# Kernel optimization log

Hardware: AMD Instinct MI355X
Metric: run time of the kernel (lower is better)

Reference implementation:

```python
import jax, jax.numpy as jnp
import numpy as np

B, T, S = 64, 256, 512          # batch, decode steps, source length
IN, H, P, C = 512, 512, 256, 512  # in_size, rnn hidden, ctx_proj_size, ctx_size


def setup_inputs() -> dict:
    key = jax.random.key(0)
    ks = jax.random.split(key, 10)
    def n(k, sh, s=0.05):
        return jax.random.normal(k, sh, dtype=jnp.float32) * s
    return {
        "dec_input": n(ks[0], (B, T, IN), 1.0),
        "ctx": n(ks[1], (B, S, C), 1.0),
        "ctx_mask": jnp.ones((B, S), jnp.float32),
        # LSTMCell layer 0: input = in_size + ctx_proj_size (input feeding)
        "Wih0": n(ks[2], (4 * H, IN + P)),
        "Whh0": n(ks[3], (4 * H, H)),
        "bih0": jnp.zeros((4 * H,), jnp.float32),
        "bhh0": jnp.zeros((4 * H,), jnp.float32),
        # LSTMCell layer 1
        "Wih1": n(ks[4], (4 * H, H)),
        "Whh1": n(ks[5], (4 * H, H)),
        "bih1": jnp.zeros((4 * H,), jnp.float32),
        "bhh1": jnp.zeros((4 * H,), jnp.float32),
        # bilinear (Luong general) attention weight
        "Watt": n(ks[6], (H, C)),
        # ctx projection: Linear(rnn_size + att.out_features -> ctx_proj_size)
        "Wproj": n(ks[7], (P, H + C)),
        "bproj": jnp.zeros((P,), jnp.float32),
    }


def _lstm_cell(x, h, c, Wih, Whh, bih, bhh):
    # PyTorch LSTMCell gate order: i, f, g, o
    g = x @ Wih.T + bih + h @ Whh.T + bhh
    i, f, gg, o = jnp.split(g, 4, axis=-1)
    c_new = jax.nn.sigmoid(f) * c + jax.nn.sigmoid(i) * jnp.tanh(gg)
    h_new = jax.nn.sigmoid(o) * jnp.tanh(c_new)
    return h_new, c_new


def reference(dec_input, ctx, ctx_mask, Wih0, Whh0, bih0, bhh0,
              Wih1, Whh1, bih1, bhh1, Watt, Wproj, bproj):
    Bn = dec_input.shape[0]
    neg = (ctx_mask - 1.0) * 1e9  # additive mask: 0 where valid, -1e9 where pad

    def step(carry, x_t):
        h0, c0, h1, c1, feed = carry
        # input feeding at layer 0
        x = jnp.concatenate([x_t, feed], axis=1)
        h0, c0 = _lstm_cell(x, h0, c0, Wih0, Whh0, bih0, bhh0)
        h1, c1 = _lstm_cell(h0, h1, c1, Wih1, Whh1, bih1, bhh1)
        # attention on last layer (att_nth_layer == -1)
        q = h1 @ Watt                                   # [B, C]
        score = jnp.einsum('bc,bsc->bs', q, ctx) + neg  # [B, S]
        alpha = jax.nn.softmax(score, axis=-1)
        ectx = jnp.einsum('bs,bsc->bc', alpha, ctx)     # expected context [B, C]
        # ctx projection with tanh (scale_src = scale_tgt = 1.0)
        res = jnp.tanh(jnp.concatenate([h1, ectx], axis=1) @ Wproj.T + bproj)
        return (h0, c0, h1, c1, res), (res, alpha)

    z = lambda d: jnp.zeros((Bn, d), jnp.float32)
    init = (z(H), z(H), z(H), z(H), z(P))
    _, (dec_out, att_w) = jax.lax.scan(step, init, jnp.swapaxes(dec_input, 0, 1))
    # dec_output [B, T, P], attention weights [B, T, S]
    return jnp.swapaxes(dec_out, 0, 1), jnp.swapaxes(att_w, 0, 1)
```

## Files before the change

### kernel.cpp

```cpp
#include <hip/hip_runtime.h>
#include <math.h>

#define B  64
#define T  256
#define S  512
#define IN 512
#define H  512
#define P  256
#define C  512

typedef _Float16 f16x8 __attribute__((ext_vector_type(8)));
typedef float    f32x4 __attribute__((ext_vector_type(4)));
typedef unsigned short u16x8 __attribute__((ext_vector_type(8)));

#define MFMA16(a, b, c) __builtin_amdgcn_mfma_f32_16x16x32_f16(a, b, c, 0, 0, 0)

#define O_C0      0
#define O_C1      131072
#define O_H0F0    262144
#define O_H1F0    524288
#define O_FEEDF   786432
#define O_H1F32   851968
#define O_XF0     983040
#define O_Q       1245184
#define O_PS      1376256
#define O_PSP     1378304
#define O_PEA     1509376
#define O_BCAT0   2557952
#define O_BCAT1   2566144
#define O_WPROJT  2574336
#define O_W0F     3622912
#define O_W1F     14108672
#define O_WATTF   22497280
#define O_CTXH    23545856
#define O_CNTA    57100288
#define O_CNT3    57104384
#define O_H0F1N   57169920
#define O_H1F1N   57300992
#define O_XF1N    57432064

__device__ __forceinline__ float sigm(float x) { return 1.f / (1.f + __expf(-x)); }

__device__ __forceinline__ void split2(float v, unsigned short& hi, unsigned short& lo)
{
    _Float16 h = (_Float16)v;
    float r = (v - (float)h) * 4096.f;
    _Float16 l2 = (_Float16)r;
    union { _Float16 f; unsigned short u; } a, b2;
    a.f = h; b2.f = l2;
    hi = a.u; lo = b2.u;
}

__device__ __forceinline__ unsigned short f2h(float v)
{
    union { _Float16 f; unsigned short u; } x;
    x.f = (_Float16)v;
    return x.u;
}

__device__ __forceinline__ float h2f(unsigned short u)
{
    union { unsigned short u; _Float16 f; } x;
    x.u = u;
    return (float)x.f;
}

__device__ __forceinline__ int frag_us(int r, int k)
{
    return ((((k >> 5) * 4 + (r >> 4)) * 64 + ((k >> 3) & 3) * 16 + (r & 15)) * 16) + (k & 7);
}

__device__ __forceinline__ void gemm_core(
    const unsigned short* A0, int n0, const unsigned short* A1, int n1,
    const unsigned short* A2, const unsigned short* Wf, int nks, int ct,
    float* red, int tid)
{
    const int l = tid & 63, kh = tid >> 6;
    f32x4 acch[4] = {};
    f32x4 accl[4] = {};
    const int KQ = nks >> 3;
#pragma unroll 2
    for (int i = 0; i < KQ; ++i) {
        const int ks = kh * KQ + i;
        const unsigned short* ap; int ksl;
        if (ks < n0)           { ap = A0; ksl = ks; }
        else if (ks < n0 + n1) { ap = A1; ksl = ks - n0; }
        else                   { ap = A2; ksl = ks - n0 - n1; }
        const f16x8 b = *(const f16x8*)(Wf + ((long)(ct * nks + ks) * 64 + l) * 8);
#pragma unroll
        for (int mt = 0; mt < 4; ++mt) {
            const f16x8* app = (const f16x8*)(ap + (((ksl * 4 + mt) * 64 + l) * 16));
            const f16x8 ah = app[0];
            const f16x8 al = app[1];
            acch[mt] = MFMA16(ah, b, acch[mt]);
            accl[mt] = MFMA16(al, b, accl[mt]);
        }
    }
#pragma unroll
    for (int mt = 0; mt < 4; ++mt) {
        f32x4 v = acch[mt] + accl[mt] * (1.f / 4096.f);
        *(f32x4*)&red[(kh * 64 + l) * 20 + mt * 4] = v;
    }
}

__device__ __forceinline__ void lstm_epi(const float* red, const float* bias,
                                         float* cbuf, unsigned short* hfrag,
                                         float* hf32_out, int ct, int tid)
{
    const int b = tid & 63, hl = tid >> 6;
    float g4[4];
#pragma unroll
    for (int g = 0; g < 4; ++g) {
        const int col = hl * 4 + g;
        const int li  = ((b & 15) >> 2) * 16 + col;
        const int ri  = (b >> 4) * 4 + (b & 3);
        float v = bias[ct * 16 + col];
#pragma unroll
        for (int k2 = 0; k2 < 8; ++k2) v += red[(k2 * 64 + li) * 20 + ri];
        g4[g] = v;
    }
    const int hg = ct * 4 + hl;
    const float cold = cbuf[b * H + hg];
    const float cn = sigm(g4[1]) * cold + sigm(g4[0]) * tanhf(g4[2]);
    cbuf[b * H + hg] = cn;
    const float hn = sigm(g4[3]) * tanhf(cn);
    unsigned short hi, lo; split2(hn, hi, lo);
    const int fu = frag_us(b, hg);
    hfrag[fu]     = hi;
    hfrag[fu + 8] = lo;
    if (hf32_out) hf32_out[b * H + hg] = hn;
}

__global__ __launch_bounds__(512)
void k1_kernel(char* __restrict__ wsb, const float* __restrict__ dec_input, int t)
{
    __shared__ float lds[10240];
    const int bid = blockIdx.x, tid = threadIdx.x;
    const int cur = t & 1, nxt = cur ^ 1;
    unsigned short* h0f[2] = {(unsigned short*)(wsb + O_H0F0), (unsigned short*)(wsb + O_H0F1N)};
    unsigned short* xf[2]  = {(unsigned short*)(wsb + O_XF0),  (unsigned short*)(wsb + O_XF1N)};

    if (bid < 128) {
        gemm_core(xf[cur], 16, (unsigned short*)(wsb + O_FEEDF), 8, h0f[cur],
                  (const unsigned short*)(wsb + O_W0F), 40, bid, lds, tid);
        __syncthreads();
        if (tid < 256)
            lstm_epi(lds, (const float*)(wsb + O_BCAT0), (float*)(wsb + O_C0),
                     h0f[nxt], nullptr, bid, tid);
    } else if (t + 1 < T) {
        const int idx = (bid - 128) * 512 + tid;
        const int bb = idx >> 9, k = idx & 511;
        unsigned short hi, lo;
        split2(dec_input[((long)bb * T + (t + 1)) * IN + k], hi, lo);
        unsigned short* dst = xf[nxt];
        const int fu = frag_us(bb, k);
        dst[fu]     = hi;
        dst[fu + 8] = lo;
    }
}

__global__ __launch_bounds__(512)
void k2_kernel(char* __restrict__ wsb, int t)
{
    __shared__ float lds[10240];
    const int bid = blockIdx.x, tid = threadIdx.x;
    const int cur = t & 1, nxt = cur ^ 1;
    unsigned short* h0f[2] = {(unsigned short*)(wsb + O_H0F0), (unsigned short*)(wsb + O_H0F1N)};
    unsigned short* h1f[2] = {(unsigned short*)(wsb + O_H1F0), (unsigned short*)(wsb + O_H1F1N)};

    gemm_core(h0f[nxt], 16, h1f[cur], 16, nullptr,
              (const unsigned short*)(wsb + O_W1F), 32, bid, lds, tid);
    __syncthreads();
    if (tid < 256)
        lstm_epi(lds, (const float*)(wsb + O_BCAT1), (float*)(wsb + O_C1),
                 h1f[nxt], (float*)(wsb + O_H1F32), bid, tid);
}

__global__ __launch_bounds__(512)
void q_kernel(char* __restrict__ wsb, int t)
{
    __shared__ float lds[10240];
    const int bid = blockIdx.x, tid = threadIdx.x;
    const int nxt = (t & 1) ^ 1;
    unsigned short* h1f[2] = {(unsigned short*)(wsb + O_H1F0), (unsigned short*)(wsb + O_H1F1N)};
    float* qbuf = (float*)(wsb + O_Q);

    gemm_core(h1f[nxt], 16, nullptr, 0, nullptr,
              (const unsigned short*)(wsb + O_WATTF), 16, bid, lds, tid);
    __syncthreads();
    if (tid < 256) {
        const int b = tid & 63, cl = tid >> 6;
        float4 vv;
#pragma unroll
        for (int c2 = 0; c2 < 4; ++c2) {
            const int col = cl * 4 + c2;
            const int li  = ((b & 15) >> 2) * 16 + col;
            const int ri  = (b >> 4) * 4 + (b & 3);
            float v = 0.f;
#pragma unroll
            for (int k2 = 0; k2 < 8; ++k2) v += lds[(k2 * 64 + li) * 20 + ri];
            ((float*)&vv)[c2] = v;
        }
        *(float4*)(qbuf + b * C + bid * 16 + cl * 4) = vv;
    }
}

__global__ __launch_bounds__(512)
void qattn_kernel(char* __restrict__ wsb, const float* __restrict__ mask, int t)
{
    __shared__ float qs[512];
    __shared__ unsigned short tile[32 * 520];
    __shared__ float scl[64];

    const int bid = blockIdx.x, tid = threadIdx.x;
    const int b = bid >> 3, ei = bid & 7;
    const float* qbuf = (const float*)(wsb + O_Q);
    const unsigned short* ctxh = (const unsigned short*)(wsb + O_CTXH);
    float* pS  = (float*)(wsb + O_PSP);
    float* Ps  = (float*)(wsb + O_PS);
    float* Pea = (float*)(wsb + O_PEA);

    const unsigned short* cb16 = ctxh + ((long)b * S + ei * 64) * C;
    u16x8 creg[4];
#pragma unroll
    for (int it = 0; it < 4; ++it)
        creg[it] = *(const u16x8*)(cb16 + (long)(it * 512 + tid) * 8);

    if (tid < 128) ((float4*)qs)[tid] = ((const float4*)(qbuf + (long)b * C))[tid];
    __syncthreads();

    const int row = tid >> 4;
    const int ch  = tid & 15;
    float qv[32];
#pragma unroll
    for (int j = 0; j < 32; ++j) qv[j] = qs[ch * 32 + j];

    float eacc = 0.f;
#pragma unroll
    for (int tt = 0; tt < 2; ++tt) {
#pragma unroll
        for (int it = 0; it < 4; ++it) {
            const int i = it * 512 + tid;
            const int r = (i >> 6) & 31, c8 = i & 63;
            *(u16x8*)&tile[r * 520 + c8 * 8] = creg[it];
        }
        __syncthreads();
        if (tt == 0) {
#pragma unroll
            for (int it = 0; it < 4; ++it)
                creg[it] = *(const u16x8*)(cb16 + 32 * 512 + (long)(it * 512 + tid) * 8);
        }
        float part = 0.f;
#pragma unroll
        for (int j4 = 0; j4 < 4; ++j4) {
            const u16x8 cv = *(const u16x8*)&tile[row * 520 + ch * 32 + j4 * 8];
#pragma unroll
            for (int m = 0; m < 8; ++m)
                part = fmaf(h2f(cv[m]), qv[j4 * 8 + m], part);
        }
        part += __shfl_xor(part, 1);
        part += __shfl_xor(part, 2);
        part += __shfl_xor(part, 4);
        part += __shfl_xor(part, 8);
        if (ch == 0) {
            const int srow = ei * 64 + tt * 32 + row;
            const float sc = part + (mask[(long)b * S + srow] - 1.f) * 1e9f;
            const float p  = __expf(sc - 20.f);
            scl[tt * 32 + row] = p;
            pS[(long)b * S + srow] = p;
        }
        __syncthreads();
#pragma unroll 8
        for (int s = 0; s < 32; ++s)
            eacc = fmaf(scl[tt * 32 + s], h2f(tile[s * 520 + tid]), eacc);
        __syncthreads();
    }

    Pea[(long)bid * 512 + tid] = eacc;
    if (tid < 64) {
        float v = scl[tid];
#pragma unroll
        for (int off = 32; off; off >>= 1) v += __shfl_xor(v, off);
        if (tid == 0) Ps[bid] = v;
    }
}

__global__ __launch_bounds__(512)
void mergeproj_kernel(char* __restrict__ wsb, const float* __restrict__ bproj,
                      float* __restrict__ out, int t)
{
    __shared__ float ectx[512];
    __shared__ float h1l[512];
    __shared__ float red[512];

    const int b = blockIdx.x, tid = threadIdx.x;
    const float* Ps  = (const float*)(wsb + O_PS);
    const float* Pea = (const float*)(wsb + O_PEA);
    const float* pS  = (const float*)(wsb + O_PSP);
    const float* h1f32 = (const float*)(wsb + O_H1F32);
    const unsigned short* Wph = (const unsigned short*)(wsb + O_WPROJT);
    unsigned short* feedf = (unsigned short*)(wsb + O_FEEDF);

    float* dec_out = out;
    float* att_out = out + (long)B * T * P;

    float gs = 0.f;
#pragma unroll
    for (int j = 0; j < 8; ++j) gs += Ps[b * 8 + j];
    const float inv = 1.f / gs;

    float v = 0.f;
#pragma unroll
    for (int j = 0; j < 8; ++j) v += Pea[(long)(b * 8 + j) * 512 + tid];
    ectx[tid] = v * inv;
    h1l[tid]  = h1f32[(long)b * H + tid];
    att_out[((long)b * T + t) * S + tid] = pS[(long)b * S + tid] * inv;
    __syncthreads();

    const int p = tid & 255, half = tid >> 8;
    const float* al = half ? ectx : h1l;
    const unsigned short* Wp = Wph + (long)(half * 512) * P + p;
    float acc = 0.f;
#pragma unroll 8
    for (int kk = 0; kk < 512; ++kk)
        acc = fmaf(al[kk], h2f(Wp[(long)kk * P]), acc);
    red[tid] = acc;
    __syncthreads();

    if (tid < 256) {
        float vv = red[tid] + red[tid + 256] + bproj[tid];
        vv = tanhf(vv);
        dec_out[((long)b * T + t) * P + tid] = vv;
        unsigned short hi, lo; split2(vv, hi, lo);
        const int fu = frag_us(b, tid);
        feedf[fu]     = hi;
        feedf[fu + 8] = lo;
    }
}

__global__ __launch_bounds__(256)
void prep_all(const float* __restrict__ dec_input,
              const float* __restrict__ Wih0, const float* __restrict__ Whh0,
              const float* __restrict__ bih0, const float* __restrict__ bhh0,
              const float* __restrict__ Wih1, const float* __restrict__ Whh1,
              const float* __restrict__ bih1, const float* __restrict__ bhh1,
              const float* __restrict__ Watt, const float* __restrict__ Wproj,
              const float* __restrict__ ctx,
              char* __restrict__ wsb)
{
    const int bid = blockIdx.x, tid = threadIdx.x;
    if (bid < 240) {
        float4 z = {0.f, 0.f, 0.f, 0.f};
        ((float4*)wsb)[bid * 256 + tid] = z;
    } else if (bid < 368) {
        const int idx = (bid - 240) * 256 + tid;
        const int bb = idx >> 9, k = idx & 511;
        unsigned short hi, lo;
        split2(dec_input[((long)bb * T) * IN + k], hi, lo);
        unsigned short* xf0 = (unsigned short*)(wsb + O_XF0);
        const int fu = frag_us(bb, k);
        xf0[fu] = hi; xf0[fu + 8] = lo;
    } else if (bid < 384) {
        const int idx = (bid - 368) * 256 + tid;
        if (idx < 2048) {
            const int p = idx, h = p >> 2, g = p & 3, orig = g * H + h;
            ((float*)(wsb + O_BCAT0))[p] = bih0[orig] + bhh0[orig];
        } else {
            const int p = idx - 2048, h = p >> 2, g = p & 3, orig = g * H + h;
            ((float*)(wsb + O_BCAT1))[p] = bih1[orig] + bhh1[orig];
        }
    } else if (bid < 512) {
        const int idx = (bid - 384) * 256 + tid;
        const int n = idx >> 6, k = (idx & 63) * 8;
        u16x8 hv;
#pragma unroll
        for (int j = 0; j < 8; ++j) hv[j] = f2h(Watt[(long)(k + j) * C + n]);
        unsigned short* Wf = (unsigned short*)(wsb + O_WATTF);
        const long base = ((long)((n >> 4) * 16 + (k >> 5)) * 64 + ((k >> 3) & 3) * 16 + (n & 15)) * 8;
        *(u16x8*)(Wf + base) = hv;
    } else if (bid < 1536) {
        const int idx = (bid - 512) * 256 + tid;
        const int k = idx >> 8, p = idx & 255;
        ((unsigned short*)(wsb + O_WPROJT))[k * P + p] = f2h(Wproj[(long)p * (H + C) + k]);
    } else if (bid < 2816) {
        const int idx = (bid - 1536) * 256 + tid;
        const int n = idx / 160, k8 = idx - n * 160;
        const int k = k8 * 8;
        const int h = n >> 2, g = n & 3, orig = g * H + h;
        const float* src = (k < IN + P) ? (Wih0 + (long)orig * (IN + P) + k)
                                        : (Whh0 + (long)orig * H + (k - (IN + P)));
        u16x8 hv;
#pragma unroll
        for (int j = 0; j < 8; ++j) hv[j] = f2h(src[j]);
        unsigned short* Wf = (unsigned short*)(wsb + O_W0F);
        const long base = ((long)((n >> 4) * 40 + (k >> 5)) * 64 + ((k >> 3) & 3) * 16 + (n & 15)) * 8;
        *(u16x8*)(Wf + base) = hv;
    } else if (bid < 3840) {
        const int idx = (bid - 2816) * 256 + tid;
        const int n = idx >> 7, k = (idx & 127) * 8;
        const int h = n >> 2, g = n & 3, orig = g * H + h;
        const float* src = (k < H) ? (Wih1 + (long)orig * H + k)
                                   : (Whh1 + (long)orig * H + (k - H));
        u16x8 hv;
#pragma unroll
        for (int j = 0; j < 8; ++j) hv[j] = f2h(src[j]);
        unsigned short* Wf = (unsigned short*)(wsb + O_W1F);
        const long base = ((long)((n >> 4) * 32 + (k >> 5)) * 64 + ((k >> 3) & 3) * 16 + (n & 15)) * 8;
        *(u16x8*)(Wf + base) = hv;
    } else if (bid < 7936) {
        const long idx = (long)(bid - 3840) * 256 + tid;
        const float* src = ctx + idx * 16;
        unsigned short* dst = (unsigned short*)(wsb + O_CTXH) + idx * 16;
        u16x8 o0, o1;
#pragma unroll
        for (int j = 0; j < 8; ++j) {
            o0[j] = f2h(src[j]);
            o1[j] = f2h(src[j + 8]);
        }
        *(u16x8*)dst       = o0;
        *(u16x8*)(dst + 8) = o1;
    } else {
        float4 z = {0.f, 0.f, 0.f, 0.f};
        ((float4*)(wsb + O_CNTA))[(bid - 7936) * 256 + tid] = z;
    }
}

extern "C" void kernel_launch(void* const* d_in, const int* in_sizes, int n_in,
                              void* d_out, int out_size, void* d_ws, size_t ws_size,
                              hipStream_t stream)
{
    (void)in_sizes; (void)n_in; (void)out_size; (void)ws_size;
    const float* dec_input = (const float*)d_in[0];
    const float* ctx       = (const float*)d_in[1];
    const float* mask      = (const float*)d_in[2];
    const float* Wih0      = (const float*)d_in[3];
    const float* Whh0      = (const float*)d_in[4];
    const float* bih0      = (const float*)d_in[5];
    const float* bhh0      = (const float*)d_in[6];
    const float* Wih1      = (const float*)d_in[7];
    const float* Whh1      = (const float*)d_in[8];
    const float* bih1      = (const float*)d_in[9];
    const float* bhh1      = (const float*)d_in[10];
    const float* Watt      = (const float*)d_in[11];
    const float* Wproj     = (const float*)d_in[12];
    const float* bproj     = (const float*)d_in[13];
    float* out = (float*)d_out;
    char*  wsb = (char*)d_ws;

    prep_all<<<7953, 256, 0, stream>>>(dec_input, Wih0, Whh0, bih0, bhh0,
                                       Wih1, Whh1, bih1, bhh1, Watt, Wproj,
                                       ctx, wsb);

    for (int t = 0; t < T; ++t) {
        k1_kernel<<<192, 512, 0, stream>>>(wsb, dec_input, t);
        k2_kernel<<<128, 512, 0, stream>>>(wsb, t);
        q_kernel<<<32, 512, 0, stream>>>(wsb, t);
        qattn_kernel<<<512, 512, 0, stream>>>(wsb, mask, t);
        mergeproj_kernel<<<64, 512, 0, stream>>>(wsb, bproj, out, t);
    }
}
```

Before: 13.92 ms.

## Precompute recurrent-independent LSTM gate partials off the critical path

```diff
diff --git a/kernel.cpp b/kernel.cpp
--- a/kernel.cpp
+++ b/kernel.cpp
@@ -30,11 +30,13 @@
 #define O_BCAT1   2566144
 #define O_WPROJT  2574336
 #define O_W0F     3622912
+#define O_PK1A    8865792
+#define O_PK1B    9390080
+#define O_PK2A    9914368
+#define O_PK2B    10438656
 #define O_W1F     14108672
 #define O_WATTF   22497280
 #define O_CTXH    23545856
-#define O_CNTA    57100288
-#define O_CNT3    57104384
 #define O_H0F1N   57169920
 #define O_H1F1N   57300992
 #define O_XF1N    57432064
@@ -72,8 +74,8 @@
 
 __device__ __forceinline__ void gemm_core(
     const unsigned short* A0, int n0, const unsigned short* A1, int n1,
-    const unsigned short* A2, const unsigned short* Wf, int nks, int ct,
-    float* red, int tid)
+    const unsigned short* A2, const unsigned short* Wf, int wnks, int wbase,
+    int nks, int ct, float* red, int tid)
 {
     const int l = tid & 63, kh = tid >> 6;
     f32x4 acch[4] = {};
@@ -86,7 +88,7 @@
         if (ks < n0)           { ap = A0; ksl = ks; }
         else if (ks < n0 + n1) { ap = A1; ksl = ks - n0; }
         else                   { ap = A2; ksl = ks - n0 - n1; }
-        const f16x8 b = *(const f16x8*)(Wf + ((long)(ct * nks + ks) * 64 + l) * 8);
+        const f16x8 b = *(const f16x8*)(Wf + ((long)(ct * wnks + wbase + ks) * 64 + l) * 8);
 #pragma unroll
         for (int mt = 0; mt < 4; ++mt) {
             const f16x8* app = (const f16x8*)(ap + (((ksl * 4 + mt) * 64 + l) * 16));
@@ -103,18 +105,35 @@
     }
 }
 
-__device__ __forceinline__ void lstm_epi(const float* red, const float* bias,
-                                         float* cbuf, unsigned short* hfrag,
-                                         float* hf32_out, int ct, int tid)
+__device__ __forceinline__ void part_store(const float* red, float* Pp,
+                                           int ct, int tid)
 {
     const int b = tid & 63, hl = tid >> 6;
-    float g4[4];
 #pragma unroll
     for (int g = 0; g < 4; ++g) {
         const int col = hl * 4 + g;
         const int li  = ((b & 15) >> 2) * 16 + col;
         const int ri  = (b >> 4) * 4 + (b & 3);
-        float v = bias[ct * 16 + col];
+        float v = 0.f;
+#pragma unroll
+        for (int k2 = 0; k2 < 8; ++k2) v += red[(k2 * 64 + li) * 20 + ri];
+        Pp[(ct * 16 + col) * 64 + b] = v;
+    }
+}
+
+__device__ __forceinline__ void lstm_epi_p(const float* red, const float* Pp,
+                                           const float* bias, float* cbuf,
+                                           unsigned short* hfrag, float* hf32_out,
+                                           int ct, int tid)
+{
+    const int b = tid & 63, hl = tid >> 6;
+    float g4[4];
+#pragma unroll
+    for (int g = 0; g < 4; ++g) {
+        const int col = hl * 4 + g;
+        const int li  = ((b & 15) >> 2) * 16 + col;
+        const int ri  = (b >> 4) * 4 + (b & 3);
+        float v = bias[ct * 16 + col] + Pp[(ct * 16 + col) * 64 + b];
 #pragma unroll
         for (int k2 = 0; k2 < 8; ++k2) v += red[(k2 * 64 + li) * 20 + ri];
         g4[g] = v;
@@ -132,48 +151,50 @@
 }
 
 __global__ __launch_bounds__(512)
-void k1_kernel(char* __restrict__ wsb, const float* __restrict__ dec_input, int t)
+void k1part0_kernel(char* __restrict__ wsb)
+{
+    __shared__ float lds[10240];
+    const int bid = blockIdx.x, tid = threadIdx.x;
+    gemm_core((unsigned short*)(wsb + O_XF0), 16,
+              (unsigned short*)(wsb + O_H0F0), 16, nullptr,
+              (const unsigned short*)(wsb + O_W0F), 40, 0, 32, bid, lds, tid);
+    __syncthreads();
+    if (tid < 256) part_store(lds, (float*)(wsb + O_PK1A), bid, tid);
+}
+
+__global__ __launch_bounds__(512)
+void k1fin_kernel(char* __restrict__ wsb, int t)
 {
     __shared__ float lds[10240];
     const int bid = blockIdx.x, tid = threadIdx.x;
     const int cur = t & 1, nxt = cur ^ 1;
     unsigned short* h0f[2] = {(unsigned short*)(wsb + O_H0F0), (unsigned short*)(wsb + O_H0F1N)};
-    unsigned short* xf[2]  = {(unsigned short*)(wsb + O_XF0),  (unsigned short*)(wsb + O_XF1N)};
-
-    if (bid < 128) {
-        gemm_core(xf[cur], 16, (unsigned short*)(wsb + O_FEEDF), 8, h0f[cur],
-                  (const unsigned short*)(wsb + O_W0F), 40, bid, lds, tid);
-        __syncthreads();
-        if (tid < 256)
-            lstm_epi(lds, (const float*)(wsb + O_BCAT0), (float*)(wsb + O_C0),
-                     h0f[nxt], nullptr, bid, tid);
-    } else if (t + 1 < T) {
-        const int idx = (bid - 128) * 512 + tid;
-        const int bb = idx >> 9, k = idx & 511;
-        unsigned short hi, lo;
-        split2(dec_input[((long)bb * T + (t + 1)) * IN + k], hi, lo);
-        unsigned short* dst = xf[nxt];
-        const int fu = frag_us(bb, k);
-        dst[fu]     = hi;
-        dst[fu + 8] = lo;
-    }
+    const float* Pk1[2] = {(const float*)(wsb + O_PK1A), (const float*)(wsb + O_PK1B)};
+
+    gemm_core((unsigned short*)(wsb + O_FEEDF), 8, nullptr, 0, nullptr,
+              (const unsigned short*)(wsb + O_W0F), 40, 32, 8, bid, lds, tid);
+    __syncthreads();
+    if (tid < 256)
+        lstm_epi_p(lds, Pk1[cur], (const float*)(wsb + O_BCAT0),
+                   (float*)(wsb + O_C0), h0f[nxt], nullptr, bid, tid);
 }
 
 __global__ __launch_bounds__(512)
-void k2_kernel(char* __restrict__ wsb, int t)
+void k2fin_kernel(char* __restrict__ wsb, int t)
 {
     __shared__ float lds[10240];
     const int bid = blockIdx.x, tid = threadIdx.x;
     const int cur = t & 1, nxt = cur ^ 1;
     unsigned short* h0f[2] = {(unsigned short*)(wsb + O_H0F0), (unsigned short*)(wsb + O_H0F1N)};
     unsigned short* h1f[2] = {(unsigned short*)(wsb + O_H1F0), (unsigned short*)(wsb + O_H1F1N)};
-
-    gemm_core(h0f[nxt], 16, h1f[cur], 16, nullptr,
-              (const unsigned short*)(wsb + O_W1F), 32, bid, lds, tid);
+    const float* Pk2[2] = {(const float*)(wsb + O_PK2A), (const float*)(wsb + O_PK2B)};
+
+    gemm_core(h0f[nxt], 16, nullptr, 0, nullptr,
+              (const unsigned short*)(wsb + O_W1F), 32, 0, 16, bid, lds, tid);
     __syncthreads();
     if (tid < 256)
-        lstm_epi(lds, (const float*)(wsb + O_BCAT1), (float*)(wsb + O_C1),
-                 h1f[nxt], (float*)(wsb + O_H1F32), bid, tid);
+        lstm_epi_p(lds, Pk2[cur], (const float*)(wsb + O_BCAT1),
+                   (float*)(wsb + O_C1), h1f[nxt], (float*)(wsb + O_H1F32), bid, tid);
 }
 
 __global__ __launch_bounds__(512)
@@ -186,7 +207,7 @@
     float* qbuf = (float*)(wsb + O_Q);
 
     gemm_core(h1f[nxt], 16, nullptr, 0, nullptr,
-              (const unsigned short*)(wsb + O_WATTF), 16, bid, lds, tid);
+              (const unsigned short*)(wsb + O_WATTF), 16, 0, 16, bid, lds, tid);
     __syncthreads();
     if (tid < 256) {
         const int b = tid & 63, cl = tid >> 6;
@@ -206,13 +227,38 @@
 }
 
 __global__ __launch_bounds__(512)
-void qattn_kernel(char* __restrict__ wsb, const float* __restrict__ mask, int t)
-{
-    __shared__ float qs[512];
-    __shared__ unsigned short tile[32 * 520];
-    __shared__ float scl[64];
-
-    const int bid = blockIdx.x, tid = threadIdx.x;
+void attn_parts_kernel(char* __restrict__ wsb, const float* __restrict__ mask, int t)
+{
+    __shared__ char smem[40960];
+    const int bid = blockIdx.x, tid = threadIdx.x;
+    const int cur = t & 1, nxt = cur ^ 1;
+
+    if (bid >= 512) {
+        if (t + 1 >= T) return;
+        float* red = (float*)smem;
+        unsigned short* h0f[2] = {(unsigned short*)(wsb + O_H0F0), (unsigned short*)(wsb + O_H0F1N)};
+        unsigned short* h1f[2] = {(unsigned short*)(wsb + O_H1F0), (unsigned short*)(wsb + O_H1F1N)};
+        unsigned short* xf[2]  = {(unsigned short*)(wsb + O_XF0),  (unsigned short*)(wsb + O_XF1N)};
+        if (bid < 640) {
+            float* Pk1[2] = {(float*)(wsb + O_PK1A), (float*)(wsb + O_PK1B)};
+            gemm_core(xf[nxt], 16, h0f[nxt], 16, nullptr,
+                      (const unsigned short*)(wsb + O_W0F), 40, 0, 32, bid - 512, red, tid);
+            __syncthreads();
+            if (tid < 256) part_store(red, Pk1[nxt], bid - 512, tid);
+        } else {
+            float* Pk2[2] = {(float*)(wsb + O_PK2A), (float*)(wsb + O_PK2B)};
+            gemm_core(h1f[nxt], 16, nullptr, 0, nullptr,
+                      (const unsigned short*)(wsb + O_W1F), 32, 16, 16, bid - 640, red, tid);
+            __syncthreads();
+            if (tid < 256) part_store(red, Pk2[nxt], bid - 640, tid);
+        }
+        return;
+    }
+
+    float* qs = (float*)smem;
+    unsigned short* tile = (unsigned short*)(smem + 2048);
+    float* scl = (float*)(smem + 35328);
+
     const int b = bid >> 3, ei = bid & 7;
     const float* qbuf = (const float*)(wsb + O_Q);
     const unsigned short* ctxh = (const unsigned short*)(wsb + O_CTXH);
@@ -286,14 +332,32 @@
 }
 
 __global__ __launch_bounds__(512)
-void mergeproj_kernel(char* __restrict__ wsb, const float* __restrict__ bproj,
-                      float* __restrict__ out, int t)
+void mp_kernel(char* __restrict__ wsb, const float* __restrict__ bproj,
+               const float* __restrict__ dec_input, float* __restrict__ out, int t)
 {
     __shared__ float ectx[512];
     __shared__ float h1l[512];
     __shared__ float red[512];
 
-    const int b = blockIdx.x, tid = threadIdx.x;
+    const int bid = blockIdx.x, tid = threadIdx.x;
+    const int cur = t & 1;
+
+    if (bid >= 64) {
+        if (t + 2 < T) {
+            unsigned short* xf[2] = {(unsigned short*)(wsb + O_XF0), (unsigned short*)(wsb + O_XF1N)};
+            const int idx = (bid - 64) * 512 + tid;
+            const int bb = idx >> 9, k = idx & 511;
+            unsigned short hi, lo;
+            split2(dec_input[((long)bb * T + (t + 2)) * IN + k], hi, lo);
+            unsigned short* dst = xf[cur];
+            const int fu = frag_us(bb, k);
+            dst[fu]     = hi;
+            dst[fu + 8] = lo;
+        }
+        return;
+    }
+
+    const int b = bid;
     const float* Ps  = (const float*)(wsb + O_PS);
     const float* Pea = (const float*)(wsb + O_PEA);
     const float* pS  = (const float*)(wsb + O_PSP);
@@ -387,8 +451,10 @@
         const int n = idx / 160, k8 = idx - n * 160;
         const int k = k8 * 8;
         const int h = n >> 2, g = n & 3, orig = g * H + h;
-        const float* src = (k < IN + P) ? (Wih0 + (long)orig * (IN + P) + k)
-                                        : (Whh0 + (long)orig * H + (k - (IN + P)));
+        const float* src;
+        if (k < 512)       src = Wih0 + (long)orig * (IN + P) + k;
+        else if (k < 1024) src = Whh0 + (long)orig * H + (k - 512);
+        else               src = Wih0 + (long)orig * (IN + P) + 512 + (k - 1024);
         u16x8 hv;
 #pragma unroll
         for (int j = 0; j < 8; ++j) hv[j] = f2h(src[j]);
@@ -419,9 +485,17 @@
         }
         *(u16x8*)dst       = o0;
         *(u16x8*)(dst + 8) = o1;
+    } else if (bid < 8064) {
+        float4 z = {0.f, 0.f, 0.f, 0.f};
+        ((float4*)(wsb + O_PK2A))[(bid - 7936) * 256 + tid] = z;
     } else {
-        float4 z = {0.f, 0.f, 0.f, 0.f};
-        ((float4*)(wsb + O_CNTA))[(bid - 7936) * 256 + tid] = z;
+        const int idx = (bid - 8064) * 256 + tid;
+        const int bb = idx >> 9, k = idx & 511;
+        unsigned short hi, lo;
+        split2(dec_input[((long)bb * T + 1) * IN + k], hi, lo);
+        unsigned short* xf1 = (unsigned short*)(wsb + O_XF1N);
+        const int fu = frag_us(bb, k);
+        xf1[fu] = hi; xf1[fu + 8] = lo;
     }
 }
 
@@ -447,15 +521,16 @@
     float* out = (float*)d_out;
     char*  wsb = (char*)d_ws;
 
-    prep_all<<<7953, 256, 0, stream>>>(dec_input, Wih0, Whh0, bih0, bhh0,
+    prep_all<<<8192, 256, 0, stream>>>(dec_input, Wih0, Whh0, bih0, bhh0,
                                        Wih1, Whh1, bih1, bhh1, Watt, Wproj,
                                        ctx, wsb);
+    k1part0_kernel<<<128, 512, 0, stream>>>(wsb);
 
     for (int t = 0; t < T; ++t) {
-        k1_kernel<<<192, 512, 0, stream>>>(wsb, dec_input, t);
-        k2_kernel<<<128, 512, 0, stream>>>(wsb, t);
+        k1fin_kernel<<<128, 512, 0, stream>>>(wsb, t);
+        k2fin_kernel<<<128, 512, 0, stream>>>(wsb, t);
         q_kernel<<<32, 512, 0, stream>>>(wsb, t);
-        qattn_kernel<<<512, 512, 0, stream>>>(wsb, mask, t);
-        mergeproj_kernel<<<64, 512, 0, stream>>>(wsb, bproj, out, t);
-    }
-}
+        attn_parts_kernel<<<768, 512, 0, stream>>>(wsb, mask, t);
+        mp_kernel<<<128, 512, 0, stream>>>(wsb, bproj, dec_input, out, t);
+    }
+}
```

After: 13.05 ms, median of 2. 1.07x faster.
